# Optimization experiments

Hardware: AMD Instinct MI355X
Metric: run time of the kernel (lower is better)

## Reference

```python
import jax, jax.numpy as jnp
import numpy as np

N_NODES = 100000
N_EDGES = 1600000
IN_FEATS, N_HIDDEN, N_CLASSES = 128, 64, 40


def setup_inputs() -> dict:
    key = jax.random.key(0)
    ks = jax.random.split(key, 6)
    h = jax.random.normal(ks[0], (N_NODES, IN_FEATS), dtype=jnp.float32)
    W0 = jax.random.normal(ks[1], (IN_FEATS, N_HIDDEN), dtype=jnp.float32) * (1.0 / np.sqrt(IN_FEATS))
    b0 = jnp.zeros((N_HIDDEN,), dtype=jnp.float32)
    W1 = jax.random.normal(ks[2], (N_HIDDEN, N_HIDDEN), dtype=jnp.float32) * (1.0 / np.sqrt(N_HIDDEN))
    b1 = jnp.zeros((N_HIDDEN,), dtype=jnp.float32)
    W2 = jax.random.normal(ks[3], (N_HIDDEN, N_CLASSES), dtype=jnp.float32) * (1.0 / np.sqrt(N_HIDDEN))
    b2 = jnp.zeros((N_CLASSES,), dtype=jnp.float32)
    src = jax.random.randint(ks[4], (N_EDGES,), 0, N_NODES, dtype=jnp.int32)
    dst = jax.random.randint(ks[5], (N_EDGES,), 0, N_NODES, dtype=jnp.int32)
    return {"h": h, "W0": W0, "b0": b0, "W1": W1, "b1": b1, "W2": W2, "b2": b2, "src": src, "dst": dst}


def _degrees(src, dst):
    ones = jnp.ones(src.shape[0], dtype=jnp.float32)
    out_deg = jax.ops.segment_sum(ones, src, num_segments=N_NODES)
    in_deg = jax.ops.segment_sum(ones, dst, num_segments=N_NODES)
    # DGL clamps degrees to >= 1 (allow_zero_in_degree)
    norm_src = jax.lax.rsqrt(jnp.maximum(out_deg, 1.0))  # [N]
    norm_dst = jax.lax.rsqrt(jnp.maximum(in_deg, 1.0))   # [N]
    return norm_src, norm_dst


def _graph_conv(x, W, b, src, dst, norm_src, norm_dst, act):
    # DGL GraphConv, norm='both': D_in^{-1/2} A^T D_out^{-1/2} (X W) + b
    xw = (x @ W) * norm_src[:, None]               # [N, out]
    agg = jax.ops.segment_sum(xw[src], dst, num_segments=N_NODES)  # gather-scatter over edges
    out = agg * norm_dst[:, None] + b
    return jax.nn.relu(out) if act else out


def reference(h, W0, b0, W1, b1, W2, b2, src, dst):
    norm_src, norm_dst = _degrees(src, dst)
    h = _graph_conv(h, W0, b0, src, dst, norm_src, norm_dst, act=True)
    # dropout layers are identity at inference
    h = _graph_conv(h, W1, b1, src, dst, norm_src, norm_dst, act=True)
    h = _graph_conv(h, W2, b2, src, dst, norm_src, norm_dst, act=False)
    return h
```

## Files before the change

### kernel.cpp

```cpp
#include <hip/hip_runtime.h>
#include <hip/hip_fp16.h>

#define N_NODES 100000
#define N_EDGES 1600000
#define ELL_W 64
#define ZROW N_NODES
#define NCHUNK 64
#define NSEG 4
#define CH (N_EDGES / NCHUNK)
#define SEGN (N_NODES / NSEG)

typedef _Float16 half8 __attribute__((ext_vector_type(8)));
typedef float floatx4 __attribute__((ext_vector_type(4)));


__global__ __launch_bounds__(512) void k_count(const int* __restrict__ src, const int* __restrict__ dst,
                                               unsigned char* __restrict__ cnt_out,
                                               unsigned char* __restrict__ cnt_in) {
    __shared__ unsigned pk[SEGN];
    const int c = blockIdx.x;
    const int lo = blockIdx.y * SEGN;
    for (int i = threadIdx.x; i < SEGN; i += 512) pk[i] = 0;
    __syncthreads();
    const int4* s4 = (const int4*)(src + c * CH);
    const int4* d4 = (const int4*)(dst + c * CH);
    for (int i = threadIdx.x; i < CH / 4; i += 512) {
        int4 s = s4[i], d = d4[i];
        unsigned a;
        a = (unsigned)(s.x - lo); if (a < SEGN) atomicAdd(&pk[a], 0x10000u);
        a = (unsigned)(s.y - lo); if (a < SEGN) atomicAdd(&pk[a], 0x10000u);
        a = (unsigned)(s.z - lo); if (a < SEGN) atomicAdd(&pk[a], 0x10000u);
        a = (unsigned)(s.w - lo); if (a < SEGN) atomicAdd(&pk[a], 0x10000u);
        a = (unsigned)(d.x - lo); if (a < SEGN) atomicAdd(&pk[a], 1u);
        a = (unsigned)(d.y - lo); if (a < SEGN) atomicAdd(&pk[a], 1u);
        a = (unsigned)(d.z - lo); if (a < SEGN) atomicAdd(&pk[a], 1u);
        a = (unsigned)(d.w - lo); if (a < SEGN) atomicAdd(&pk[a], 1u);
    }
    __syncthreads();
    for (int i = threadIdx.x; i < SEGN; i += 512) {
        unsigned v = pk[i];
        cnt_in [c * N_NODES + lo + i] = (unsigned char)(v & 0xFFFF);
        cnt_out[c * N_NODES + lo + i] = (unsigned char)(v >> 16);
    }
}

__global__ __launch_bounds__(256) void k_scan(unsigned char* __restrict__ cnt_in,
                                              const unsigned char* __restrict__ cnt_out,
                                              int* __restrict__ fill, float* __restrict__ norm_src,
                                              float* __restrict__ norm_dst) {
    int d = blockIdx.x * 256 + threadIdx.x;
    if (d >= N_NODES) return;
    int run = 0;
    for (int c = 0; c < NCHUNK; ++c) {
        int v = cnt_in[c * N_NODES + d];
        cnt_in[c * N_NODES + d] = (unsigned char)run;
        run += v;
    }
    int od = 0;
    for (int c = 0; c < NCHUNK; ++c) od += cnt_out[c * N_NODES + d];
    fill[d] = run;
    norm_dst[d] = rsqrtf((float)(run < 1 ? 1 : run));
    norm_src[d] = rsqrtf((float)(od  < 1 ? 1 : od ));
}

__global__ __launch_bounds__(512) void k_scatter(const int* __restrict__ src, const int* __restrict__ dst,
                                                 const unsigned char* __restrict__ bases,
                                                 int* __restrict__ ell,
                                                 __half* __restrict__ padA, __half* __restrict__ padB,
                                                 __half* __restrict__ padC) {
    __shared__ unsigned base[SEGN / 2];
    const int c = blockIdx.x;
    const int lo = blockIdx.y * SEGN;
    if (c == 0 && blockIdx.y == 0) {
        int t = threadIdx.x;
        if (t < 32)                { ((unsigned*)(padA + (size_t)N_NODES * 64))[t]      = 0u; }
        else if (t < 64)           { ((unsigned*)(padB + (size_t)N_NODES * 64))[t - 32] = 0u; }
        else if (t < 84)           { ((unsigned*)(padC + (size_t)N_NODES * 40))[t - 64] = 0u; }
    }
    for (int i = threadIdx.x; i < SEGN / 2; i += 512) {
        unsigned b0 = bases[c * N_NODES + lo + 2 * i];
        unsigned b1 = bases[c * N_NODES + lo + 2 * i + 1];
        base[i] = b0 | (b1 << 16);
    }
    __syncthreads();
    const int4* s4 = (const int4*)(src + c * CH);
    const int4* d4 = (const int4*)(dst + c * CH);
    for (int i = threadIdx.x; i < CH / 4; i += 512) {
        int4 s = s4[i], d = d4[i];
        unsigned r, sh, old; int p;
        r = (unsigned)(d.x - lo); if (r < SEGN) { sh = (r & 1) << 4; old = atomicAdd(&base[r >> 1], 1u << sh); p = (old >> sh) & 0xFFFF; if (p < ELL_W) ell[p * N_NODES + lo + r] = s.x; }
        r = (unsigned)(d.y - lo); if (r < SEGN) { sh = (r & 1) << 4; old = atomicAdd(&base[r >> 1], 1u << sh); p = (old >> sh) & 0xFFFF; if (p < ELL_W) ell[p * N_NODES + lo + r] = s.y; }
        r = (unsigned)(d.z - lo); if (r < SEGN) { sh = (r & 1) << 4; old = atomicAdd(&base[r >> 1], 1u << sh); p = (old >> sh) & 0xFFFF; if (p < ELL_W) ell[p * N_NODES + lo + r] = s.z; }
        r = (unsigned)(d.w - lo); if (r < SEGN) { sh = (r & 1) << 4; old = atomicAdd(&base[r >> 1], 1u << sh); p = (old >> sh) & 0xFFFF; if (p < ELL_W) ell[p * N_NODES + lo + r] = s.w; }
    }
}

__device__ __forceinline__ void acc16B(const float4& v, float* acc) {
    const __half2* hh = (const __half2*)&v;
    #pragma unroll
    for (int t = 0; t < 4; ++t) {
        float2 f = __half22float2(hh[t]);
        acc[2 * t + 0] += f.x;
        acc[2 * t + 1] += f.y;
    }
}

template<int KK>
__device__ __forceinline__ void loadb8(float4* V, const __half* __restrict__ base,
                                       const int* __restrict__ idxr, int b, int q) {
    #pragma unroll
    for (int u = 0; u < 8; ++u)
        V[u] = *(const float4*)(base + (long)idxr[b + u] * KK + q * 8);
}

__device__ __forceinline__ void accb8(const float4* V, float* acc) {
    #pragma unroll
    for (int u = 0; u < 8; ++u) acc16B(V[u], acc);
}

template<int KK>
__device__ __forceinline__ void gather_row(float* acc, const __half* __restrict__ XW,
                                           const int* __restrict__ idxr, int dg, int q) {
    int nb = (dg + 7) >> 3;
    if (nb <= 0) return;
    float4 va[8], vb[8];
    loadb8<KK>(va, XW, idxr, 0, q);
    int it = 1;
    for (; it + 1 < nb; it += 2) {
        loadb8<KK>(vb, XW, idxr, it * 8, q);
        accb8(va, acc);
        loadb8<KK>(va, XW, idxr, (it + 1) * 8, q);
        accb8(vb, acc);
    }
    if (it < nb) {
        loadb8<KK>(vb, XW, idxr, it * 8, q);
        accb8(va, acc);
        accb8(vb, acc);
    } else {
        accb8(va, acc);
    }
}

template<int K, int NCOL>
__global__ __launch_bounds__(256) void k_gemm(const float* __restrict__ Xv, const float* __restrict__ W,
                                              const float* __restrict__ norm, __half* __restrict__ Y) {
    constexpr int NT = (NCOL + 15) / 16;
    constexpr int NR = NT * 16;
    __shared__ __align__(16) _Float16 Xh[64][K + 8];
    __shared__ __align__(16) _Float16 Wt[NR][K + 8];
    const int tid = threadIdx.x;
    const int row0 = blockIdx.x * 64;

    for (int idx = tid; idx < K * NCOL; idx += 256) {
        int k = idx / NCOL, c = idx - (idx / NCOL) * NCOL;
        Wt[c][k] = (_Float16)W[idx];
    }
    for (int idx = tid; idx < (NR - NCOL) * K; idx += 256) {
        int c = NCOL + idx / K, k = idx - (idx / K) * K;
        Wt[c][k] = (_Float16)0;
    }

    for (int idx = tid; idx < 64 * (K / 8); idx += 256) {
        int r = idx / (K / 8), kc = idx - (idx / (K / 8)) * (K / 8);
        int gr = row0 + r;
        half8 v = {0, 0, 0, 0, 0, 0, 0, 0};
        if (gr < N_NODES) {
            const float* X = Xv + (long)gr * K + kc * 8;
            float4 u0 = *(const float4*)(X + 0);
            float4 u1 = *(const float4*)(X + 4);
            v.s0 = (_Float16)u0.x; v.s1 = (_Float16)u0.y;
            v.s2 = (_Float16)u0.z; v.s3 = (_Float16)u0.w;
            v.s4 = (_Float16)u1.x; v.s5 = (_Float16)u1.y;
            v.s6 = (_Float16)u1.z; v.s7 = (_Float16)u1.w;
        }
        *(half8*)&Xh[r][kc * 8] = v;
    }
    __syncthreads();

    const int lane = tid & 63;
    const int wave = tid >> 6;
    const int quad = lane >> 4;
    const int l16 = lane & 15;
    const int r0 = wave * 16;

    floatx4 acc[NT] = {};
    #pragma unroll
    for (int k0 = 0; k0 < K; k0 += 32) {
        half8 a = *(const half8*)&Xh[r0 + l16][k0 + quad * 8];
        #pragma unroll
        for (int t = 0; t < NT; ++t) {
            half8 b = *(const half8*)&Wt[t * 16 + l16][k0 + quad * 8];
            acc[t] = __builtin_amdgcn_mfma_f32_16x16x32_f16(a, b, acc[t], 0, 0, 0);
        }
    }

    #pragma unroll
    for (int i = 0; i < 4; ++i) {
        int gr = row0 + r0 + quad * 4 + i;
        if (gr < N_NODES) {
            float s = norm[gr];
            #pragma unroll
            for (int t = 0; t < NT; ++t) {
                int c = t * 16 + l16;
                if (c < NCOL) Y[(long)gr * NCOL + c] = __float2half(acc[t][i] * s);
            }
        }
    }
}

template<int K, int NCOL>
__global__ __launch_bounds__(512, 4) void k_agg_gemm(const __half* __restrict__ XWp, const int* __restrict__ ell,
                                                     const int* __restrict__ deg, const float* __restrict__ norm_dst,
                                                     const float* __restrict__ biasp, const float* __restrict__ W,
                                                     const float* __restrict__ norm, __half* __restrict__ Y) {
    constexpr int NT = (NCOL + 15) / 16;
    constexpr int NR = NT * 16;
    __shared__ __align__(16) _Float16 Xh[64][K + 8];
    __shared__ __align__(16) _Float16 Wt[NR][K + 8];
    __shared__ int sIdx[64][68];
    __shared__ int sDeg[64];
    __shared__ int sMax;
    const int tid = threadIdx.x;
    const int row0 = blockIdx.x * 64;

    for (int idx = tid; idx < K * NCOL; idx += 512) {
        int k = idx / NCOL, c = idx - (idx / NCOL) * NCOL;
        Wt[c][k] = (_Float16)W[idx];
    }
    for (int idx = tid; idx < (NR - NCOL) * K; idx += 512) {
        int c = NCOL + idx / K, k = idx - (idx / K) * K;
        Wt[c][k] = (_Float16)0;
    }

    if (tid < 64) {
        int node = row0 + tid;
        int dg = 0;
        if (node < N_NODES) { dg = deg[node]; if (dg > ELL_W) dg = ELL_W; }
        sDeg[tid] = dg;
        int v = dg;
        #pragma unroll
        for (int o = 32; o > 0; o >>= 1) v = max(v, __shfl_down(v, o));
        if (tid == 0) sMax = v;
    }
    __syncthreads();
    const int mpad = (sMax + 7) & ~7;
    for (int i = tid; i < mpad * 64; i += 512) {
        int slot = i >> 6, r = i & 63;
        int node = row0 + r;
        sIdx[r][slot] = (node < N_NODES && slot < sDeg[r]) ? ell[slot * N_NODES + node] : ZROW;
    }
    __syncthreads();

    {
        int r = tid >> 3, q = tid & 7;
        int d = row0 + r;
        int dg = sDeg[r];
        const int* idxr = sIdx[r];
        float acc[8] = {};
        gather_row<K>(acc, XWp, idxr, dg, q);
        _Float16 res[8] = {};
        if (d < N_NODES) {
            float nd = norm_dst[d];
            #pragma unroll
            for (int t = 0; t < 8; ++t) {
                float o = acc[t] * nd + biasp[q * 8 + t];
                res[t] = (_Float16)fmaxf(o, 0.f);
            }
        }
        *(half8*)&Xh[r][q * 8] = *(const half8*)res;
    }
    __syncthreads();

    const int lane = tid & 63;
    const int wave = tid >> 6;
    if (wave < 4) {
        const int quad = lane >> 4;
        const int l16 = lane & 15;
        const int r0 = wave * 16;

        floatx4 acc[NT] = {};
        #pragma unroll
        for (int k0 = 0; k0 < K; k0 += 32) {
            half8 a = *(const half8*)&Xh[r0 + l16][k0 + quad * 8];
            #pragma unroll
            for (int t = 0; t < NT; ++t) {
                half8 b = *(const half8*)&Wt[t * 16 + l16][k0 + quad * 8];
                acc[t] = __builtin_amdgcn_mfma_f32_16x16x32_f16(a, b, acc[t], 0, 0, 0);
            }
        }

        #pragma unroll
        for (int i = 0; i < 4; ++i) {
            int gr = row0 + r0 + quad * 4 + i;
            if (gr < N_NODES) {
                float s = norm[gr];
                #pragma unroll
                for (int t = 0; t < NT; ++t) {
                    int c = t * 16 + l16;
                    if (c < NCOL) Y[(long)gr * NCOL + c] = __float2half(acc[t][i] * s);
                }
            }
        }
    }
}

template<int NF>
__global__ __launch_bounds__(320, 4) void k_agg_f(const __half* __restrict__ XW, const int* __restrict__ ell,
                                                  const int* __restrict__ deg, const float* __restrict__ norm_dst,
                                                  const float* __restrict__ bias, float* __restrict__ OUT) {
    constexpr int NQ = NF / 8;
    __shared__ int sIdx[64][68];
    __shared__ int sDeg[64];
    __shared__ int sMax;
    const int tid = threadIdx.x;
    const int row0 = blockIdx.x * 64;

    if (tid < 64) {
        int node = row0 + tid;
        int dg = 0;
        if (node < N_NODES) { dg = deg[node]; if (dg > ELL_W) dg = ELL_W; }
        sDeg[tid] = dg;
        int v = dg;
        #pragma unroll
        for (int o = 32; o > 0; o >>= 1) v = max(v, __shfl_down(v, o));
        if (tid == 0) sMax = v;
    }
    __syncthreads();
    const int mpad = (sMax + 7) & ~7;
    for (int i = tid; i < mpad * 64; i += 320) {
        int slot = i >> 6, r = i & 63;
        int node = row0 + r;
        sIdx[r][slot] = (node < N_NODES && slot < sDeg[r]) ? ell[slot * N_NODES + node] : ZROW;
    }
    __syncthreads();

    const int r = tid / NQ, q = tid - (tid / NQ) * NQ;
    const int d = row0 + r;
    if (d >= N_NODES) return;
    const int dg = sDeg[r];
    const int* idxr = sIdx[r];

    float acc[8] = {};
    gather_row<NF>(acc, XW, idxr, dg, q);

    float nd = norm_dst[d];
    float o[8];
    #pragma unroll
    for (int t = 0; t < 8; ++t) o[t] = acc[t] * nd + bias[q * 8 + t];
    *(float4*)(OUT + (long)d * NF + q * 8 + 0) = make_float4(o[0], o[1], o[2], o[3]);
    *(float4*)(OUT + (long)d * NF + q * 8 + 4) = make_float4(o[4], o[5], o[6], o[7]);
}

extern "C" void kernel_launch(void* const* d_in, const int* in_sizes, int n_in,
                              void* d_out, int out_size, void* d_ws, size_t ws_size,
                              hipStream_t stream) {
    const float* h  = (const float*)d_in[0];
    const float* W0 = (const float*)d_in[1];
    const float* b0 = (const float*)d_in[2];
    const float* W1 = (const float*)d_in[3];
    const float* b1 = (const float*)d_in[4];
    const float* W2 = (const float*)d_in[5];
    const float* b2 = (const float*)d_in[6];
    const int* src  = (const int*)d_in[7];
    const int* dst  = (const int*)d_in[8];
    float* out = (float*)d_out;

    char* ws = (char*)d_ws;
    size_t off = 0;
    int* fill        = (int*)(ws + off); off += (size_t)N_NODES * 4;
    float* norm_src  = (float*)(ws + off); off += (size_t)N_NODES * 4;
    float* norm_dst  = (float*)(ws + off); off += (size_t)N_NODES * 4;
    int* ell         = (int*)(ws + off); off += (size_t)N_NODES * ELL_W * 4;
    unsigned char* cnt_in  = (unsigned char*)(ws + off);
    __half* bufC = (__half*)(ws + off); off += (size_t)NCHUNK * N_NODES;
    unsigned char* cnt_out = (unsigned char*)(ws + off); off += (size_t)NCHUNK * N_NODES;
    __half* bufA  = (__half*)(ws + off); off += (size_t)(N_NODES + 1) * 64 * 2;
    __half* bufB  = (__half*)(ws + off); off += (size_t)(N_NODES + 1) * 64 * 2;

    k_count<<<dim3(NCHUNK, NSEG), 512, 0, stream>>>(src, dst, cnt_out, cnt_in);
    k_scan<<<(N_NODES + 255) / 256, 256, 0, stream>>>(cnt_in, cnt_out, fill, norm_src, norm_dst);
    k_scatter<<<dim3(NCHUNK, NSEG), 512, 0, stream>>>(src, dst, cnt_in, ell, bufA, bufB, bufC);

    const int grid = (N_NODES + 63) / 64;

    k_gemm<128, 64><<<grid, 256, 0, stream>>>(h, W0, norm_src, bufA);
    k_agg_gemm<64, 64><<<grid, 512, 0, stream>>>(bufA, ell, fill, norm_dst, b0, W1, norm_src, bufB);
    k_agg_gemm<64, 40><<<grid, 512, 0, stream>>>(bufB, ell, fill, norm_dst, b1, W2, norm_src, bufC);
    k_agg_f<40><<<grid, 320, 0, stream>>>(bufC, ell, fill, norm_dst, b2, out);
}
```

Baseline: 279.4 us.

## Order ELL neighbor slots by source-node range to improve gather locality

The in-degree counting now keeps four 8-bit sub-counters per destination, one per quarter of the source-node range, and the scan builds per-range offsets. As a result the scatter writes each destination's neighbors into ELL slots grouped by source range, and out-degree counts move to a separate packed shared buffer. The aim is more locality in the later gathers over feature rows, at the cost of wider 32-bit count arrays and the workspace reshuffle this requires. Padding-row zeroing moves into the first GEMM because bufA and bufC now alias the count buffer; the 8-bit sub-counters could overflow if more than 255 edges fall into one bucket.

```diff
diff --git a/kernel.cpp b/kernel.cpp
--- a/kernel.cpp
+++ b/kernel.cpp
@@ -9,6 +9,7 @@
 #define NSEG 4
 #define CH (N_EDGES / NCHUNK)
 #define SEGN (N_NODES / NSEG)
+#define RDIV 25000u
 
 typedef _Float16 half8 __attribute__((ext_vector_type(8)));
 typedef float floatx4 __attribute__((ext_vector_type(4)));
@@ -16,82 +17,81 @@
 
 __global__ __launch_bounds__(512) void k_count(const int* __restrict__ src, const int* __restrict__ dst,
                                                unsigned char* __restrict__ cnt_out,
-                                               unsigned char* __restrict__ cnt_in) {
-    __shared__ unsigned pk[SEGN];
+                                               unsigned* __restrict__ cnt_in4) {
+    __shared__ unsigned pkIn[SEGN];
+    __shared__ unsigned pkOut[SEGN / 4];
     const int c = blockIdx.x;
     const int lo = blockIdx.y * SEGN;
-    for (int i = threadIdx.x; i < SEGN; i += 512) pk[i] = 0;
+    for (int i = threadIdx.x; i < SEGN; i += 512) pkIn[i] = 0;
+    for (int i = threadIdx.x; i < SEGN / 4; i += 512) pkOut[i] = 0;
     __syncthreads();
     const int4* s4 = (const int4*)(src + c * CH);
     const int4* d4 = (const int4*)(dst + c * CH);
     for (int i = threadIdx.x; i < CH / 4; i += 512) {
         int4 s = s4[i], d = d4[i];
         unsigned a;
-        a = (unsigned)(s.x - lo); if (a < SEGN) atomicAdd(&pk[a], 0x10000u);
-        a = (unsigned)(s.y - lo); if (a < SEGN) atomicAdd(&pk[a], 0x10000u);
-        a = (unsigned)(s.z - lo); if (a < SEGN) atomicAdd(&pk[a], 0x10000u);
-        a = (unsigned)(s.w - lo); if (a < SEGN) atomicAdd(&pk[a], 0x10000u);
-        a = (unsigned)(d.x - lo); if (a < SEGN) atomicAdd(&pk[a], 1u);
-        a = (unsigned)(d.y - lo); if (a < SEGN) atomicAdd(&pk[a], 1u);
-        a = (unsigned)(d.z - lo); if (a < SEGN) atomicAdd(&pk[a], 1u);
-        a = (unsigned)(d.w - lo); if (a < SEGN) atomicAdd(&pk[a], 1u);
+        a = (unsigned)(s.x - lo); if (a < SEGN) atomicAdd(&pkOut[a >> 2], 1u << ((a & 3) * 8));
+        a = (unsigned)(s.y - lo); if (a < SEGN) atomicAdd(&pkOut[a >> 2], 1u << ((a & 3) * 8));
+        a = (unsigned)(s.z - lo); if (a < SEGN) atomicAdd(&pkOut[a >> 2], 1u << ((a & 3) * 8));
+        a = (unsigned)(s.w - lo); if (a < SEGN) atomicAdd(&pkOut[a >> 2], 1u << ((a & 3) * 8));
+        a = (unsigned)(d.x - lo); if (a < SEGN) atomicAdd(&pkIn[a], 1u << (((unsigned)s.x / RDIV) * 8));
+        a = (unsigned)(d.y - lo); if (a < SEGN) atomicAdd(&pkIn[a], 1u << (((unsigned)s.y / RDIV) * 8));
+        a = (unsigned)(d.z - lo); if (a < SEGN) atomicAdd(&pkIn[a], 1u << (((unsigned)s.z / RDIV) * 8));
+        a = (unsigned)(d.w - lo); if (a < SEGN) atomicAdd(&pkIn[a], 1u << (((unsigned)s.w / RDIV) * 8));
     }
     __syncthreads();
     for (int i = threadIdx.x; i < SEGN; i += 512) {
-        unsigned v = pk[i];
-        cnt_in [c * N_NODES + lo + i] = (unsigned char)(v & 0xFFFF);
-        cnt_out[c * N_NODES + lo + i] = (unsigned char)(v >> 16);
-    }
-}
-
-__global__ __launch_bounds__(256) void k_scan(unsigned char* __restrict__ cnt_in,
+        cnt_in4[(size_t)c * N_NODES + lo + i] = pkIn[i];
+        cnt_out[(size_t)c * N_NODES + lo + i] = (unsigned char)((pkOut[i >> 2] >> ((i & 3) * 8)) & 0xFF);
+    }
+}
+
+__global__ __launch_bounds__(256) void k_scan(unsigned* __restrict__ cnt_in4,
                                               const unsigned char* __restrict__ cnt_out,
                                               int* __restrict__ fill, float* __restrict__ norm_src,
                                               float* __restrict__ norm_dst) {
     int d = blockIdx.x * 256 + threadIdx.x;
     if (d >= N_NODES) return;
-    int run = 0;
+    unsigned v[NCHUNK];
+    unsigned dr0 = 0, dr1 = 0, dr2 = 0, dr3 = 0;
+    #pragma unroll
     for (int c = 0; c < NCHUNK; ++c) {
-        int v = cnt_in[c * N_NODES + d];
-        cnt_in[c * N_NODES + d] = (unsigned char)run;
-        run += v;
+        v[c] = cnt_in4[(size_t)c * N_NODES + d];
+        dr0 += v[c] & 0xFF; dr1 += (v[c] >> 8) & 0xFF;
+        dr2 += (v[c] >> 16) & 0xFF; dr3 += v[c] >> 24;
+    }
+    unsigned run = dr0 + dr1 + dr2 + dr3;
+    unsigned roff = (dr0 << 8) | ((dr0 + dr1) << 16) | ((dr0 + dr1 + dr2) << 24);
+    #pragma unroll
+    for (int c = 0; c < NCHUNK; ++c) {
+        cnt_in4[(size_t)c * N_NODES + d] = roff;
+        roff += v[c];
     }
     int od = 0;
-    for (int c = 0; c < NCHUNK; ++c) od += cnt_out[c * N_NODES + d];
-    fill[d] = run;
+    for (int c = 0; c < NCHUNK; ++c) od += cnt_out[(size_t)c * N_NODES + d];
+    fill[d] = (int)run;
     norm_dst[d] = rsqrtf((float)(run < 1 ? 1 : run));
     norm_src[d] = rsqrtf((float)(od  < 1 ? 1 : od ));
 }
 
 __global__ __launch_bounds__(512) void k_scatter(const int* __restrict__ src, const int* __restrict__ dst,
-                                                 const unsigned char* __restrict__ bases,
-                                                 int* __restrict__ ell,
-                                                 __half* __restrict__ padA, __half* __restrict__ padB,
-                                                 __half* __restrict__ padC) {
-    __shared__ unsigned base[SEGN / 2];
+                                                 const unsigned* __restrict__ bases4,
+                                                 int* __restrict__ ell) {
+    __shared__ unsigned base4[SEGN];
     const int c = blockIdx.x;
     const int lo = blockIdx.y * SEGN;
-    if (c == 0 && blockIdx.y == 0) {
-        int t = threadIdx.x;
-        if (t < 32)                { ((unsigned*)(padA + (size_t)N_NODES * 64))[t]      = 0u; }
-        else if (t < 64)           { ((unsigned*)(padB + (size_t)N_NODES * 64))[t - 32] = 0u; }
-        else if (t < 84)           { ((unsigned*)(padC + (size_t)N_NODES * 40))[t - 64] = 0u; }
-    }
-    for (int i = threadIdx.x; i < SEGN / 2; i += 512) {
-        unsigned b0 = bases[c * N_NODES + lo + 2 * i];
-        unsigned b1 = bases[c * N_NODES + lo + 2 * i + 1];
-        base[i] = b0 | (b1 << 16);
-    }
+    for (int i = threadIdx.x; i < SEGN; i += 512)
+        base4[i] = bases4[(size_t)c * N_NODES + lo + i];
     __syncthreads();
     const int4* s4 = (const int4*)(src + c * CH);
     const int4* d4 = (const int4*)(dst + c * CH);
     for (int i = threadIdx.x; i < CH / 4; i += 512) {
         int4 s = s4[i], d = d4[i];
         unsigned r, sh, old; int p;
-        r = (unsigned)(d.x - lo); if (r < SEGN) { sh = (r & 1) << 4; old = atomicAdd(&base[r >> 1], 1u << sh); p = (old >> sh) & 0xFFFF; if (p < ELL_W) ell[p * N_NODES + lo + r] = s.x; }
-        r = (unsigned)(d.y - lo); if (r < SEGN) { sh = (r & 1) << 4; old = atomicAdd(&base[r >> 1], 1u << sh); p = (old >> sh) & 0xFFFF; if (p < ELL_W) ell[p * N_NODES + lo + r] = s.y; }
-        r = (unsigned)(d.z - lo); if (r < SEGN) { sh = (r & 1) << 4; old = atomicAdd(&base[r >> 1], 1u << sh); p = (old >> sh) & 0xFFFF; if (p < ELL_W) ell[p * N_NODES + lo + r] = s.z; }
-        r = (unsigned)(d.w - lo); if (r < SEGN) { sh = (r & 1) << 4; old = atomicAdd(&base[r >> 1], 1u << sh); p = (old >> sh) & 0xFFFF; if (p < ELL_W) ell[p * N_NODES + lo + r] = s.w; }
+        r = (unsigned)(d.x - lo); if (r < SEGN) { sh = ((unsigned)s.x / RDIV) * 8; old = atomicAdd(&base4[r], 1u << sh); p = (old >> sh) & 0xFF; if (p < ELL_W) ell[p * N_NODES + lo + r] = s.x; }
+        r = (unsigned)(d.y - lo); if (r < SEGN) { sh = ((unsigned)s.y / RDIV) * 8; old = atomicAdd(&base4[r], 1u << sh); p = (old >> sh) & 0xFF; if (p < ELL_W) ell[p * N_NODES + lo + r] = s.y; }
+        r = (unsigned)(d.z - lo); if (r < SEGN) { sh = ((unsigned)s.z / RDIV) * 8; old = atomicAdd(&base4[r], 1u << sh); p = (old >> sh) & 0xFF; if (p < ELL_W) ell[p * N_NODES + lo + r] = s.z; }
+        r = (unsigned)(d.w - lo); if (r < SEGN) { sh = ((unsigned)s.w / RDIV) * 8; old = atomicAdd(&base4[r], 1u << sh); p = (old >> sh) & 0xFF; if (p < ELL_W) ell[p * N_NODES + lo + r] = s.w; }
     }
 }
 
@@ -143,13 +143,20 @@
 
 template<int K, int NCOL>
 __global__ __launch_bounds__(256) void k_gemm(const float* __restrict__ Xv, const float* __restrict__ W,
-                                              const float* __restrict__ norm, __half* __restrict__ Y) {
+                                              const float* __restrict__ norm, __half* __restrict__ Y,
+                                              __half* __restrict__ padB, __half* __restrict__ padC) {
     constexpr int NT = (NCOL + 15) / 16;
     constexpr int NR = NT * 16;
     __shared__ __align__(16) _Float16 Xh[64][K + 8];
     __shared__ __align__(16) _Float16 Wt[NR][K + 8];
     const int tid = threadIdx.x;
     const int row0 = blockIdx.x * 64;
+
+    if (blockIdx.x == 0) {
+        if (tid < 32)       { ((unsigned*)(Y    + (size_t)N_NODES * 64))[tid]      = 0u; }
+        else if (tid < 64)  { ((unsigned*)(padB + (size_t)N_NODES * 64))[tid - 32] = 0u; }
+        else if (tid < 84)  { ((unsigned*)(padC + (size_t)N_NODES * 40))[tid - 64] = 0u; }
+    }
 
     for (int idx = tid; idx < K * NCOL; idx += 256) {
         int k = idx / NCOL, c = idx - (idx / NCOL) * NCOL;
@@ -371,19 +378,20 @@
     float* norm_src  = (float*)(ws + off); off += (size_t)N_NODES * 4;
     float* norm_dst  = (float*)(ws + off); off += (size_t)N_NODES * 4;
     int* ell         = (int*)(ws + off); off += (size_t)N_NODES * ELL_W * 4;
-    unsigned char* cnt_in  = (unsigned char*)(ws + off);
-    __half* bufC = (__half*)(ws + off); off += (size_t)NCHUNK * N_NODES;
+    unsigned* cnt_in4 = (unsigned*)(ws + off);
+    __half* bufA = (__half*)(ws + off);
+    __half* bufC = (__half*)(ws + off + 13000000);
+    off += (size_t)NCHUNK * N_NODES * 4;
     unsigned char* cnt_out = (unsigned char*)(ws + off); off += (size_t)NCHUNK * N_NODES;
-    __half* bufA  = (__half*)(ws + off); off += (size_t)(N_NODES + 1) * 64 * 2;
     __half* bufB  = (__half*)(ws + off); off += (size_t)(N_NODES + 1) * 64 * 2;
 
-    k_count<<<dim3(NCHUNK, NSEG), 512, 0, stream>>>(src, dst, cnt_out, cnt_in);
-    k_scan<<<(N_NODES + 255) / 256, 256, 0, stream>>>(cnt_in, cnt_out, fill, norm_src, norm_dst);
-    k_scatter<<<dim3(NCHUNK, NSEG), 512, 0, stream>>>(src, dst, cnt_in, ell, bufA, bufB, bufC);
+    k_count<<<dim3(NCHUNK, NSEG), 512, 0, stream>>>(src, dst, cnt_out, cnt_in4);
+    k_scan<<<(N_NODES + 255) / 256, 256, 0, stream>>>(cnt_in4, cnt_out, fill, norm_src, norm_dst);
+    k_scatter<<<dim3(NCHUNK, NSEG), 512, 0, stream>>>(src, dst, cnt_in4, ell);
 
     const int grid = (N_NODES + 63) / 64;
 
-    k_gemm<128, 64><<<grid, 256, 0, stream>>>(h, W0, norm_src, bufA);
+    k_gemm<128, 64><<<grid, 256, 0, stream>>>(h, W0, norm_src, bufA, bufB, bufC);
     k_agg_gemm<64, 64><<<grid, 512, 0, stream>>>(bufA, ell, fill, norm_dst, b0, W1, norm_src, bufB);
     k_agg_gemm<64, 40><<<grid, 512, 0, stream>>>(bufB, ell, fill, norm_dst, b1, W2, norm_src, bufC);
     k_agg_f<40><<<grid, 320, 0, stream>>>(bufC, ell, fill, norm_dst, b2, out);
```

Result: slower. 286.7 us (+2.6%).

## Build ELL adjacency with global atomics instead of chunked count-scan-scatter

Applied to the files above, without the earlier changes.

Replaces the three-pass chunked build (per-chunk shared-memory counts, a per-node scan over 64 chunks, then a scatter) with a zero kernel, one edge-parallel kernel using global atomics for out-degree and ELL slot cursors, and a norm kernel. This removes the byte-count arrays and the serial 64-step scan per node. In exchange, slot order within a row becomes nondeterministic and the build relies on global atomic throughput. The third-layer buffer is also padded to a 64-half row stride, which aligns rows but gathers more bytes per row.

```diff
diff --git a/kernel.cpp b/kernel.cpp
--- a/kernel.cpp
+++ b/kernel.cpp
@@ -5,94 +5,51 @@
 #define N_EDGES 1600000
 #define ELL_W 64
 #define ZROW N_NODES
-#define NCHUNK 64
-#define NSEG 4
-#define CH (N_EDGES / NCHUNK)
-#define SEGN (N_NODES / NSEG)
 
 typedef _Float16 half8 __attribute__((ext_vector_type(8)));
 typedef float floatx4 __attribute__((ext_vector_type(4)));
 
 
-__global__ __launch_bounds__(512) void k_count(const int* __restrict__ src, const int* __restrict__ dst,
-                                               unsigned char* __restrict__ cnt_out,
-                                               unsigned char* __restrict__ cnt_in) {
-    __shared__ unsigned pk[SEGN];
-    const int c = blockIdx.x;
-    const int lo = blockIdx.y * SEGN;
-    for (int i = threadIdx.x; i < SEGN; i += 512) pk[i] = 0;
-    __syncthreads();
-    const int4* s4 = (const int4*)(src + c * CH);
-    const int4* d4 = (const int4*)(dst + c * CH);
-    for (int i = threadIdx.x; i < CH / 4; i += 512) {
-        int4 s = s4[i], d = d4[i];
-        unsigned a;
-        a = (unsigned)(s.x - lo); if (a < SEGN) atomicAdd(&pk[a], 0x10000u);
-        a = (unsigned)(s.y - lo); if (a < SEGN) atomicAdd(&pk[a], 0x10000u);
-        a = (unsigned)(s.z - lo); if (a < SEGN) atomicAdd(&pk[a], 0x10000u);
-        a = (unsigned)(s.w - lo); if (a < SEGN) atomicAdd(&pk[a], 0x10000u);
-        a = (unsigned)(d.x - lo); if (a < SEGN) atomicAdd(&pk[a], 1u);
-        a = (unsigned)(d.y - lo); if (a < SEGN) atomicAdd(&pk[a], 1u);
-        a = (unsigned)(d.z - lo); if (a < SEGN) atomicAdd(&pk[a], 1u);
-        a = (unsigned)(d.w - lo); if (a < SEGN) atomicAdd(&pk[a], 1u);
-    }
-    __syncthreads();
-    for (int i = threadIdx.x; i < SEGN; i += 512) {
-        unsigned v = pk[i];
-        cnt_in [c * N_NODES + lo + i] = (unsigned char)(v & 0xFFFF);
-        cnt_out[c * N_NODES + lo + i] = (unsigned char)(v >> 16);
-    }
-}
-
-__global__ __launch_bounds__(256) void k_scan(unsigned char* __restrict__ cnt_in,
-                                              const unsigned char* __restrict__ cnt_out,
-                                              int* __restrict__ fill, float* __restrict__ norm_src,
-                                              float* __restrict__ norm_dst) {
+__global__ __launch_bounds__(256) void k_zero(int* __restrict__ out_deg, int* __restrict__ cursor,
+                                              __half* __restrict__ padA, __half* __restrict__ padB,
+                                              __half* __restrict__ padC) {
+    int i = blockIdx.x * 256 + threadIdx.x;
+    int stride = gridDim.x * 256;
+    for (int j = i; j < N_NODES; j += stride) { out_deg[j] = 0; cursor[j] = 0; }
+    if (blockIdx.x == 0) {
+        int t = threadIdx.x;
+        if (t < 32)       ((unsigned*)(padA + (size_t)N_NODES * 64))[t]      = 0u;
+        else if (t < 64)  ((unsigned*)(padB + (size_t)N_NODES * 64))[t - 32] = 0u;
+        else if (t < 96)  ((unsigned*)(padC + (size_t)N_NODES * 64))[t - 64] = 0u;
+    }
+}
+
+__global__ __launch_bounds__(256) void k_build(const int* __restrict__ src, const int* __restrict__ dst,
+                                               int* __restrict__ out_deg, int* __restrict__ cursor,
+                                               int* __restrict__ ell) {
+    int i = blockIdx.x * 256 + threadIdx.x;
+    if (i >= N_EDGES / 4) return;
+    int4 s = ((const int4*)src)[i];
+    int4 d = ((const int4*)dst)[i];
+    atomicAdd(&out_deg[s.x], 1);
+    atomicAdd(&out_deg[s.y], 1);
+    atomicAdd(&out_deg[s.z], 1);
+    atomicAdd(&out_deg[s.w], 1);
+    int p;
+    p = atomicAdd(&cursor[d.x], 1); if (p < ELL_W) ell[p * N_NODES + d.x] = s.x;
+    p = atomicAdd(&cursor[d.y], 1); if (p < ELL_W) ell[p * N_NODES + d.y] = s.y;
+    p = atomicAdd(&cursor[d.z], 1); if (p < ELL_W) ell[p * N_NODES + d.z] = s.z;
+    p = atomicAdd(&cursor[d.w], 1); if (p < ELL_W) ell[p * N_NODES + d.w] = s.w;
+}
+
+__global__ __launch_bounds__(256) void k_norm(const int* __restrict__ cursor, const int* __restrict__ out_deg,
+                                              float* __restrict__ norm_src, float* __restrict__ norm_dst) {
     int d = blockIdx.x * 256 + threadIdx.x;
     if (d >= N_NODES) return;
-    int run = 0;
-    for (int c = 0; c < NCHUNK; ++c) {
-        int v = cnt_in[c * N_NODES + d];
-        cnt_in[c * N_NODES + d] = (unsigned char)run;
-        run += v;
-    }
-    int od = 0;
-    for (int c = 0; c < NCHUNK; ++c) od += cnt_out[c * N_NODES + d];
-    fill[d] = run;
+    int run = cursor[d];
+    int od = out_deg[d];
     norm_dst[d] = rsqrtf((float)(run < 1 ? 1 : run));
     norm_src[d] = rsqrtf((float)(od  < 1 ? 1 : od ));
-}
-
-__global__ __launch_bounds__(512) void k_scatter(const int* __restrict__ src, const int* __restrict__ dst,
-                                                 const unsigned char* __restrict__ bases,
-                                                 int* __restrict__ ell,
-                                                 __half* __restrict__ padA, __half* __restrict__ padB,
-                                                 __half* __restrict__ padC) {
-    __shared__ unsigned base[SEGN / 2];
-    const int c = blockIdx.x;
-    const int lo = blockIdx.y * SEGN;
-    if (c == 0 && blockIdx.y == 0) {
-        int t = threadIdx.x;
-        if (t < 32)                { ((unsigned*)(padA + (size_t)N_NODES * 64))[t]      = 0u; }
-        else if (t < 64)           { ((unsigned*)(padB + (size_t)N_NODES * 64))[t - 32] = 0u; }
-        else if (t < 84)           { ((unsigned*)(padC + (size_t)N_NODES * 40))[t - 64] = 0u; }
-    }
-    for (int i = threadIdx.x; i < SEGN / 2; i += 512) {
-        unsigned b0 = bases[c * N_NODES + lo + 2 * i];
-        unsigned b1 = bases[c * N_NODES + lo + 2 * i + 1];
-        base[i] = b0 | (b1 << 16);
-    }
-    __syncthreads();
-    const int4* s4 = (const int4*)(src + c * CH);
-    const int4* d4 = (const int4*)(dst + c * CH);
-    for (int i = threadIdx.x; i < CH / 4; i += 512) {
-        int4 s = s4[i], d = d4[i];
-        unsigned r, sh, old; int p;
-        r = (unsigned)(d.x - lo); if (r < SEGN) { sh = (r & 1) << 4; old = atomicAdd(&base[r >> 1], 1u << sh); p = (old >> sh) & 0xFFFF; if (p < ELL_W) ell[p * N_NODES + lo + r] = s.x; }
-        r = (unsigned)(d.y - lo); if (r < SEGN) { sh = (r & 1) << 4; old = atomicAdd(&base[r >> 1], 1u << sh); p = (old >> sh) & 0xFFFF; if (p < ELL_W) ell[p * N_NODES + lo + r] = s.y; }
-        r = (unsigned)(d.z - lo); if (r < SEGN) { sh = (r & 1) << 4; old = atomicAdd(&base[r >> 1], 1u << sh); p = (old >> sh) & 0xFFFF; if (p < ELL_W) ell[p * N_NODES + lo + r] = s.z; }
-        r = (unsigned)(d.w - lo); if (r < SEGN) { sh = (r & 1) << 4; old = atomicAdd(&base[r >> 1], 1u << sh); p = (old >> sh) & 0xFFFF; if (p < ELL_W) ell[p * N_NODES + lo + r] = s.w; }
-    }
 }
 
 __device__ __forceinline__ void acc16B(const float4& v, float* acc) {
@@ -208,7 +165,7 @@
     }
 }
 
-template<int K, int NCOL>
+template<int K, int NCOL, int YS>
 __global__ __launch_bounds__(512, 4) void k_agg_gemm(const __half* __restrict__ XWp, const int* __restrict__ ell,
                                                      const int* __restrict__ deg, const float* __restrict__ norm_dst,
                                                      const float* __restrict__ biasp, const float* __restrict__ W,
@@ -297,14 +254,14 @@
                 #pragma unroll
                 for (int t = 0; t < NT; ++t) {
                     int c = t * 16 + l16;
-                    if (c < NCOL) Y[(long)gr * NCOL + c] = __float2half(acc[t][i] * s);
+                    if (c < NCOL) Y[(long)gr * YS + c] = __float2half(acc[t][i] * s);
                 }
             }
         }
     }
 }
 
-template<int NF>
+template<int NF, int XS>
 __global__ __launch_bounds__(320, 4) void k_agg_f(const __half* __restrict__ XW, const int* __restrict__ ell,
                                                   const int* __restrict__ deg, const float* __restrict__ norm_dst,
                                                   const float* __restrict__ bias, float* __restrict__ OUT) {
@@ -341,7 +298,7 @@
     const int* idxr = sIdx[r];
 
     float acc[8] = {};
-    gather_row<NF>(acc, XW, idxr, dg, q);
+    gather_row<XS>(acc, XW, idxr, dg, q);
 
     float nd = norm_dst[d];
     float o[8];
@@ -367,24 +324,23 @@
 
     char* ws = (char*)d_ws;
     size_t off = 0;
-    int* fill        = (int*)(ws + off); off += (size_t)N_NODES * 4;
     float* norm_src  = (float*)(ws + off); off += (size_t)N_NODES * 4;
     float* norm_dst  = (float*)(ws + off); off += (size_t)N_NODES * 4;
+    int* out_deg     = (int*)(ws + off); off += (size_t)N_NODES * 4;
+    int* cursor      = (int*)(ws + off); off += (size_t)N_NODES * 4;
     int* ell         = (int*)(ws + off); off += (size_t)N_NODES * ELL_W * 4;
-    unsigned char* cnt_in  = (unsigned char*)(ws + off);
-    __half* bufC = (__half*)(ws + off); off += (size_t)NCHUNK * N_NODES;
-    unsigned char* cnt_out = (unsigned char*)(ws + off); off += (size_t)NCHUNK * N_NODES;
     __half* bufA  = (__half*)(ws + off); off += (size_t)(N_NODES + 1) * 64 * 2;
     __half* bufB  = (__half*)(ws + off); off += (size_t)(N_NODES + 1) * 64 * 2;
-
-    k_count<<<dim3(NCHUNK, NSEG), 512, 0, stream>>>(src, dst, cnt_out, cnt_in);
-    k_scan<<<(N_NODES + 255) / 256, 256, 0, stream>>>(cnt_in, cnt_out, fill, norm_src, norm_dst);
-    k_scatter<<<dim3(NCHUNK, NSEG), 512, 0, stream>>>(src, dst, cnt_in, ell, bufA, bufB, bufC);
+    __half* bufC  = (__half*)(ws + off); off += (size_t)(N_NODES + 1) * 64 * 2;
+
+    k_zero<<<391, 256, 0, stream>>>(out_deg, cursor, bufA, bufB, bufC);
+    k_build<<<(N_EDGES / 4 + 255) / 256, 256, 0, stream>>>(src, dst, out_deg, cursor, ell);
+    k_norm<<<(N_NODES + 255) / 256, 256, 0, stream>>>(cursor, out_deg, norm_src, norm_dst);
 
     const int grid = (N_NODES + 63) / 64;
 
     k_gemm<128, 64><<<grid, 256, 0, stream>>>(h, W0, norm_src, bufA);
-    k_agg_gemm<64, 64><<<grid, 512, 0, stream>>>(bufA, ell, fill, norm_dst, b0, W1, norm_src, bufB);
-    k_agg_gemm<64, 40><<<grid, 512, 0, stream>>>(bufB, ell, fill, norm_dst, b1, W2, norm_src, bufC);
-    k_agg_f<40><<<grid, 320, 0, stream>>>(bufC, ell, fill, norm_dst, b2, out);
-}
+    k_agg_gemm<64, 64, 64><<<grid, 512, 0, stream>>>(bufA, ell, cursor, norm_dst, b0, W1, norm_src, bufB);
+    k_agg_gemm<64, 40, 64><<<grid, 512, 0, stream>>>(bufB, ell, cursor, norm_dst, b1, W2, norm_src, bufC);
+    k_agg_f<40, 64><<<grid, 320, 0, stream>>>(bufC, ell, cursor, norm_dst, b2, out);
+}
```

Result: slower. 386.6 us (+38.3%).
